# Kernel optimization log

Measured on AMD Instinct MI355X. Metric: run time of the kernel, lower is better.

The kernel has to match this reference:

```python
import jax, jax.numpy as jnp
import numpy as np

_GROUP_SIZES = [4096, 2048, 1024, 8192, 512, 3072, 6144, 1024]
_K = 2048
_N = 2048


def setup_inputs() -> dict:
    key = jax.random.key(0)
    keys = jax.random.split(key, len(_GROUP_SIZES) + 1)
    inp = {}
    for i, m in enumerate(_GROUP_SIZES):
        inp[f"A{i}"] = jax.random.normal(keys[i], (m, _K), dtype=jnp.float32)
    inp["B_shared"] = jax.random.normal(keys[-1], (_K, _N), dtype=jnp.float32)
    return inp


def reference(A0, A1, A2, A3, A4, A5, A6, A7, B_shared):
    # torch: cat([a @ B for a in group_A], dim=0)
    # Concatenating ragged groups first and doing one GEMM is the same math
    # (row-block structure of matmul), expressed as a single fused contraction.
    A_cat = jnp.concatenate([A0, A1, A2, A3, A4, A5, A6, A7], axis=0)  # [M_total, K]
    return A_cat @ B_shared  # [M_total, N]
```

## Files before the change

kernel.cpp:

```cpp
#include <hip/hip_runtime.h>
#include <hip/hip_bf16.h>

using short8  = __attribute__((ext_vector_type(8))) short;
using ushort8 = __attribute__((ext_vector_type(8))) unsigned short;
using f32x4   = __attribute__((ext_vector_type(4))) float;

#define GLB(p)  ((const __attribute__((address_space(1))) void*)(p))
#define LDSP(p) ((__attribute__((address_space(3))) void*)(p))

static __device__ __forceinline__ unsigned short f2bf(float f) {
    union { float f; unsigned u; } v; v.f = f;
    unsigned u = v.u;
    u += 0x7fffu + ((u >> 16) & 1u);
    return (unsigned short)(u >> 16);
}

#define K_DIM 2048
#define N_DIM 2048
#define M_TOTAL 26112
#define N_GROUPS 8

__global__ __launch_bounds__(256) void cvt_all(
        const float* __restrict__ A0, const float* __restrict__ A1,
        const float* __restrict__ A2, const float* __restrict__ A3,
        const float* __restrict__ A4, const float* __restrict__ A5,
        const float* __restrict__ A6, const float* __restrict__ A7,
        const float* __restrict__ B,
        unsigned short* __restrict__ Acat, unsigned short* __restrict__ Bt) {
    int b   = blockIdx.x;
    int tid = threadIdx.x;
    if (b < 4096) {
        __shared__ float t[32][33];
        int bx = b & 63, by = b >> 6;
        int tx = tid & 31, ty = tid >> 5;
#pragma unroll
        for (int i = 0; i < 32; i += 8)
            t[ty + i][tx] = B[(long)(by * 32 + ty + i) * N_DIM + bx * 32 + tx];
        __syncthreads();
#pragma unroll
        for (int i = 0; i < 32; i += 8)
            Bt[(long)(bx * 32 + ty + i) * K_DIM + by * 32 + tx] = f2bf(t[tx][ty + i]);
    } else {
        int ab = b - 4096;
        const float* src; int gb;
        if      (ab < 256)  { src = A0; gb = 0;    }
        else if (ab < 384)  { src = A1; gb = 256;  }
        else if (ab < 448)  { src = A2; gb = 384;  }
        else if (ab < 960)  { src = A3; gb = 448;  }
        else if (ab < 992)  { src = A4; gb = 960;  }
        else if (ab < 1184) { src = A5; gb = 992;  }
        else if (ab < 1568) { src = A6; gb = 1184; }
        else                { src = A7; gb = 1568; }
        const float* s    = src  + (long)(ab - gb) * 16 * K_DIM;
        unsigned short* d = Acat + (long)ab * 16 * K_DIM;
#pragma unroll 4
        for (int i = 0; i < 16; ++i) {
            long off = (long)i * K_DIM + tid * 8;
            float4 x = *(const float4*)(s + off);
            float4 y = *(const float4*)(s + off + 4);
            ushort8 o;
            o[0] = f2bf(x.x); o[1] = f2bf(x.y); o[2] = f2bf(x.z); o[3] = f2bf(x.w);
            o[4] = f2bf(y.x); o[5] = f2bf(y.y); o[6] = f2bf(y.z); o[7] = f2bf(y.w);
            *(ushort8*)(d + off) = o;
        }
    }
}


#define PBAR() __builtin_amdgcn_s_barrier()
#define VMC(n)  asm volatile("s_waitcnt vmcnt(" #n ")" ::: "memory")

#define ST_A(BUF, H, L, TT)                                                        \
    __builtin_amdgcn_global_load_lds(                                              \
        GLB(aSt + (long)((H) * 128 + (L) * 64) * K_DIM + (TT) * 64),               \
        LDSP(lds + (BUF) * 32768 + (H) * 8192 + (L) * 4096 + w * 512), 16, 0, 0)
#define ST_B(BUF, H, L, TT)                                                        \
    __builtin_amdgcn_global_load_lds(                                              \
        GLB(bSt + (long)((H) * 128 + (L) * 64) * K_DIM + (TT) * 64),               \
        LDSP(lds + (BUF) * 32768 + 16384 + (H) * 8192 + (L) * 4096 + w * 512), 16, 0, 0)

#define MMQ(MH, NH, AV, BV)                                                        \
    _Pragma("unroll") for (int i = 0; i < 4; ++i)                                  \
    _Pragma("unroll") for (int j = 0; j < 2; ++j)                                  \
        acc[(MH) * 4 + i][(NH) * 2 + j] = __builtin_amdgcn_mfma_f32_16x16x32_bf16( \
            AV[i], BV[j], acc[(MH) * 4 + i][(NH) * 2 + j], 0, 0, 0);

#define TILE(BUF, T, DO1, DO2)                                                          \
    do {                                                                                \
        const unsigned short* pA = lds + (BUF) * 32768 + wm * 1024 + r16 * 64;          \
        const unsigned short* pB = lds + (BUF) * 32768 + 16384 + wn * 1024 + r16 * 64;  \
        short8 a0[4], a1[4], b00[2], b01[2], b10[2], b11[2];                            \
           \
        _Pragma("unroll") for (int i = 0; i < 4; ++i) {                                 \
            a0[i] = *(const short8*)(pA + i * 2048 + c0 * 8);                           \
            a1[i] = *(const short8*)(pA + i * 2048 + c1 * 8);                           \
        }                                                                               \
        _Pragma("unroll") for (int j = 0; j < 2; ++j) {                                 \
            b00[j] = *(const short8*)(pB + j * 4096 + c0 * 8);                          \
            b01[j] = *(const short8*)(pB + j * 4096 + c1 * 8);                          \
        }                                                                               \
        if (DO1) { ST_A((BUF) ^ 1, 1, 0, (T) + 1); ST_A((BUF) ^ 1, 1, 1, (T) + 1); }    \
        __builtin_amdgcn_s_setprio(1); MMQ(0, 0, a0, b00); MMQ(0, 0, a1, b01);          \
        __builtin_amdgcn_s_setprio(0); PBAR();                                          \
             \
        _Pragma("unroll") for (int j = 0; j < 2; ++j) {                                 \
            b10[j] = *(const short8*)(pB + 8192 + j * 4096 + c0 * 8);                   \
            b11[j] = *(const short8*)(pB + 8192 + j * 4096 + c1 * 8);                   \
        }                                                                               \
        if (DO2) { ST_A((BUF), 0, 0, (T) + 2); ST_A((BUF), 0, 1, (T) + 2); }            \
        __builtin_amdgcn_s_setprio(1); MMQ(0, 1, a0, b10); MMQ(0, 1, a1, b11);          \
        __builtin_amdgcn_s_setprio(0); PBAR();                                          \
                        \
        _Pragma("unroll") for (int i = 0; i < 4; ++i) {                                 \
            a0[i] = *(const short8*)(pA + 8192 + i * 2048 + c0 * 8);                    \
            a1[i] = *(const short8*)(pA + 8192 + i * 2048 + c1 * 8);                    \
        }                                                                               \
        if (DO2) { ST_B((BUF), 0, 0, (T) + 2); ST_B((BUF), 0, 1, (T) + 2); }            \
        __builtin_amdgcn_s_setprio(1); MMQ(1, 0, a0, b00); MMQ(1, 0, a1, b01);          \
        __builtin_amdgcn_s_setprio(0); PBAR();                                          \
               \
        if (DO2) { ST_B((BUF), 1, 0, (T) + 2); ST_B((BUF), 1, 1, (T) + 2); VMC(6); }    \
        __builtin_amdgcn_s_setprio(1); MMQ(1, 1, a0, b10); MMQ(1, 1, a1, b11);          \
        __builtin_amdgcn_s_setprio(0);                                                  \
    } while (0)

#define ST_A4(BUF, TT)                                                             \
    __builtin_amdgcn_global_load_lds(                                              \
        GLB(aSt + (long)(TT) * 64),                                                \
        LDSP(lds + (BUF) * 4096 + w * 512), 16, 0, 0)
#define ST_B4(BUF, H, L, TT)                                                       \
    __builtin_amdgcn_global_load_lds(                                              \
        GLB(bSt + (long)((H) * 128 + (L) * 64) * K_DIM + (TT) * 64),               \
        LDSP(lds + 8192 + (BUF) * 16384 + (H) * 8192 + (L) * 4096 + w * 512), 16, 0, 0)

#define MMQ4(NH, AV, BV)                                                           \
    _Pragma("unroll") for (int i = 0; i < 2; ++i)                                  \
    _Pragma("unroll") for (int j = 0; j < 2; ++j)                                  \
        acc[i][(NH) * 2 + j] = __builtin_amdgcn_mfma_f32_16x16x32_bf16(            \
            AV[i], BV[j], acc[i][(NH) * 2 + j], 0, 0, 0);

#define TILE64(BUF, T, DO2)                                                             \
    do {                                                                                \
        const unsigned short* pA = lds + (BUF) * 4096 + wm * 1024 + r16 * 64;           \
        const unsigned short* pB = lds + 8192 + (BUF) * 16384 + wn * 1024 + r16 * 64;   \
        short8 a0[2], a1[2], b00[2], b01[2], b10[2], b11[2];                            \
                                       \
        _Pragma("unroll") for (int i = 0; i < 2; ++i) {                                 \
            a0[i] = *(const short8*)(pA + i * 2048 + c0 * 8);                           \
            a1[i] = *(const short8*)(pA + i * 2048 + c1 * 8);                           \
        }                                                                               \
        _Pragma("unroll") for (int j = 0; j < 2; ++j) {                                 \
            b00[j] = *(const short8*)(pB + j * 4096 + c0 * 8);                          \
            b01[j] = *(const short8*)(pB + j * 4096 + c1 * 8);                          \
        }                                                                               \
        __builtin_amdgcn_s_setprio(1); MMQ4(0, a0, b00);                                \
        __builtin_amdgcn_s_setprio(0); PBAR();                                          \
                                                              \
        _Pragma("unroll") for (int j = 0; j < 2; ++j) {                                 \
            b10[j] = *(const short8*)(pB + 8192 + j * 4096 + c0 * 8);                   \
            b11[j] = *(const short8*)(pB + 8192 + j * 4096 + c1 * 8);                   \
        }                                                                               \
        __builtin_amdgcn_s_setprio(1); MMQ4(0, a1, b01);                                \
        __builtin_amdgcn_s_setprio(0); PBAR();                                          \
                                         \
        if (DO2) { ST_B4((BUF), 0, 0, (T) + 2); ST_B4((BUF), 0, 1, (T) + 2); }          \
        __builtin_amdgcn_s_setprio(1); MMQ4(1, a0, b10);                                \
        __builtin_amdgcn_s_setprio(0); PBAR();                                          \
            \
        if (DO2) { ST_B4((BUF), 1, 0, (T) + 2); ST_B4((BUF), 1, 1, (T) + 2);            \
                   ST_A4((BUF), (T) + 2); VMC(5); }                                     \
        __builtin_amdgcn_s_setprio(1); MMQ4(1, a1, b11);                                \
        __builtin_amdgcn_s_setprio(0);                                                  \
    } while (0)

__global__ __launch_bounds__(512, 2) void gemm8_kernel(const unsigned short* __restrict__ Acat,
                                                       const unsigned short* __restrict__ Bt,
                                                       float* __restrict__ C) {
    __shared__ unsigned short lds[65536];

    int wg  = blockIdx.x;
    int tid = threadIdx.x;
    int l   = tid & 63;
    int w   = tid >> 6;
    int wm  = w >> 2;
    int wn  = w & 3;
    int r16 = l & 15, kq = l >> 4, x = l & 7;
    int c0  = kq ^ x;
    int c1  = (4 + kq) ^ x;
    int srow = tid >> 3;
    int sq   = (tid & 7) ^ (srow & 7);

    if (wg < 768) {
        int swz = (wg & 7) * 102 + (wg >> 3);
        int mt  = swz >> 3, nt = swz & 7;
        int m0  = mt * 256, n0 = nt * 256;

        const unsigned short* aSt = Acat + (long)(m0 + srow) * K_DIM + sq * 8;
        const unsigned short* bSt = Bt   + (long)(n0 + srow) * K_DIM + sq * 8;

        f32x4 acc[8][4] = {};

        ST_A(0, 0, 0, 0); ST_A(0, 0, 1, 0); ST_A(0, 1, 0, 0); ST_A(0, 1, 1, 0);
        ST_B(0, 0, 0, 0); ST_B(0, 0, 1, 0); ST_B(0, 1, 0, 0); ST_B(0, 1, 1, 0);
        ST_A(1, 0, 0, 1); ST_A(1, 0, 1, 1);
        ST_B(1, 0, 0, 1); ST_B(1, 0, 1, 1); ST_B(1, 1, 0, 1); ST_B(1, 1, 1, 1);
        VMC(6); PBAR();

#pragma unroll 1
        for (int t = 0; t < 30; t += 2) {
            TILE(0, t, 1, 1);     PBAR();
            TILE(1, t + 1, 1, 1); PBAR();
        }
        TILE(0, 30, 1, 0); VMC(0); PBAR();
        TILE(1, 31, 0, 0);

        int orow = m0 + wm * 16 + (l >> 4) * 4;
        int ocol = n0 + wn * 16 + (l & 15);
#pragma unroll
        for (int i = 0; i < 8; ++i)
#pragma unroll
            for (int j = 0; j < 4; ++j)
#pragma unroll
                for (int q = 0; q < 4; ++q)
                    C[(long)(orow + i * 32 + q) * N_DIM + (ocol + j * 64)] = acc[i][j][q];
    } else {
        int k    = wg - 768;
        int o    = 768 + (k >> 2);
        int qh   = k & 3;
        int swz  = (o & 7) * 102 + (o >> 3);
        int mt   = swz >> 3, nt = swz & 7;
        int m0   = mt * 256 + qh * 64, n0 = nt * 256;

        const unsigned short* aSt = Acat + (long)(m0 + srow) * K_DIM + sq * 8;
        const unsigned short* bSt = Bt   + (long)(n0 + srow) * K_DIM + sq * 8;

        f32x4 acc[2][4] = {};

        ST_A4(0, 0);
        ST_B4(0, 0, 0, 0); ST_B4(0, 0, 1, 0); ST_B4(0, 1, 0, 0); ST_B4(0, 1, 1, 0);
        ST_A4(1, 1);
        ST_B4(1, 0, 0, 1); ST_B4(1, 0, 1, 1); ST_B4(1, 1, 0, 1); ST_B4(1, 1, 1, 1);
        VMC(5); PBAR();

#pragma unroll 1
        for (int t = 0; t < 30; ++t) {
            TILE64(t & 1, t, 1); PBAR();
        }
        TILE64(0, 30, 0); VMC(0); PBAR();
        TILE64(1, 31, 0);

        int orow = m0 + wm * 16 + (l >> 4) * 4;
        int ocol = n0 + wn * 16 + (l & 15);
#pragma unroll
        for (int i = 0; i < 2; ++i)
#pragma unroll
            for (int j = 0; j < 4; ++j)
#pragma unroll
                for (int q = 0; q < 4; ++q)
                    C[(long)(orow + i * 32 + q) * N_DIM + (ocol + j * 64)] = acc[i][j][q];
    }
}

__global__ void naive_gemm_kernel(const float* __restrict__ A, const float* __restrict__ B,
                                  float* __restrict__ C, int M) {
    __shared__ float As[16][16];
    __shared__ float Bs[16][17];
    int tx = threadIdx.x, ty = threadIdx.y;
    int row = blockIdx.y * 16 + ty;
    int col = blockIdx.x * 16 + tx;
    float s = 0.f;
    for (int k0 = 0; k0 < K_DIM; k0 += 16) {
        As[ty][tx] = A[(long)row * K_DIM + k0 + tx];
        Bs[ty][tx] = B[(long)(k0 + ty) * N_DIM + col];
        __syncthreads();
#pragma unroll
        for (int t = 0; t < 16; ++t) s += As[ty][t] * Bs[t][tx];
        __syncthreads();
    }
    C[(long)row * N_DIM + col] = s;
}

extern "C" void kernel_launch(void* const* d_in, const int* in_sizes, int n_in,
                              void* d_out, int out_size, void* d_ws, size_t ws_size,
                              hipStream_t stream) {
    static const int g_m[N_GROUPS]   = {4096, 2048, 1024, 8192, 512, 3072, 6144, 1024};
    static const int g_off[N_GROUPS] = {0, 4096, 6144, 7168, 15360, 15872, 18944, 25088};

    float* C = (float*)d_out;
    const size_t need = ((size_t)M_TOTAL * K_DIM + (size_t)N_DIM * K_DIM) * 2;

    if (ws_size >= need) {
        unsigned short* Acat = (unsigned short*)d_ws;
        unsigned short* Bt   = Acat + (size_t)M_TOTAL * K_DIM;

        cvt_all<<<4096 + M_TOTAL / 16, 256, 0, stream>>>(
            (const float*)d_in[0], (const float*)d_in[1], (const float*)d_in[2],
            (const float*)d_in[3], (const float*)d_in[4], (const float*)d_in[5],
            (const float*)d_in[6], (const float*)d_in[7], (const float*)d_in[8],
            Acat, Bt);

        gemm8_kernel<<<768 + 192, 512, 0, stream>>>(Acat, Bt, C);
    } else {
        for (int g = 0; g < N_GROUPS; ++g)
            naive_gemm_kernel<<<dim3(N_DIM / 16, g_m[g] / 16), dim3(16, 16), 0, stream>>>(
                (const float*)d_in[g], (const float*)d_in[8], C + (size_t)g_off[g] * N_DIM,
                g_m[g]);
    }
}
```

Before: 275.5 us.

## Collapse GEMM tile phases from four to two with explicit vmcnt waits

Restructures the per-K-tile schedule in both the 256x256 and 64x256 GEMM paths. Each tile now runs two compute phases instead of four, with all B fragment LDS reads hoisted up front and the next-tile global->LDS prefetches batched together. Explicit s_waitcnt vmcnt values are placed per phase instead of one wait at the end. This drops intra-tile barriers to cut synchronisation overhead, at the cost of more live registers, larger load bursts, and a risk that the new wait counts do not cover LDS buffer reuse correctly.

Result: no change. 278.1 us (+0.9%).

```diff
diff --git a/kernel.cpp b/kernel.cpp
--- a/kernel.cpp
+++ b/kernel.cpp
@@ -68,7 +68,9 @@
 
 
 #define PBAR() __builtin_amdgcn_s_barrier()
-#define VMC(n)  asm volatile("s_waitcnt vmcnt(" #n ")" ::: "memory")
+#define VMC_(n) asm volatile("s_waitcnt vmcnt(" #n ")" ::: "memory")
+#define VMCX(n) VMC_(n)
+#define VMC(n)  VMC_(n)
 
 #define ST_A(BUF, H, L, TT)                                                        \
     __builtin_amdgcn_global_load_lds(                                              \
@@ -85,12 +87,12 @@
         acc[(MH) * 4 + i][(NH) * 2 + j] = __builtin_amdgcn_mfma_f32_16x16x32_bf16( \
             AV[i], BV[j], acc[(MH) * 4 + i][(NH) * 2 + j], 0, 0, 0);
 
-#define TILE(BUF, T, DO1, DO2)                                                          \
+#define TILE2(BUF, T, DO1, DO2, VA, VB)                                                 \
     do {                                                                                \
         const unsigned short* pA = lds + (BUF) * 32768 + wm * 1024 + r16 * 64;          \
         const unsigned short* pB = lds + (BUF) * 32768 + 16384 + wn * 1024 + r16 * 64;  \
         short8 a0[4], a1[4], b00[2], b01[2], b10[2], b11[2];                            \
-           \
+          \
         _Pragma("unroll") for (int i = 0; i < 4; ++i) {                                 \
             a0[i] = *(const short8*)(pA + i * 2048 + c0 * 8);                           \
             a1[i] = *(const short8*)(pA + i * 2048 + c1 * 8);                           \
@@ -98,29 +100,29 @@
         _Pragma("unroll") for (int j = 0; j < 2; ++j) {                                 \
             b00[j] = *(const short8*)(pB + j * 4096 + c0 * 8);                          \
             b01[j] = *(const short8*)(pB + j * 4096 + c1 * 8);                          \
-        }                                                                               \
-        if (DO1) { ST_A((BUF) ^ 1, 1, 0, (T) + 1); ST_A((BUF) ^ 1, 1, 1, (T) + 1); }    \
-        __builtin_amdgcn_s_setprio(1); MMQ(0, 0, a0, b00); MMQ(0, 0, a1, b01);          \
-        __builtin_amdgcn_s_setprio(0); PBAR();                                          \
-             \
-        _Pragma("unroll") for (int j = 0; j < 2; ++j) {                                 \
             b10[j] = *(const short8*)(pB + 8192 + j * 4096 + c0 * 8);                   \
             b11[j] = *(const short8*)(pB + 8192 + j * 4096 + c1 * 8);                   \
         }                                                                               \
-        if (DO2) { ST_A((BUF), 0, 0, (T) + 2); ST_A((BUF), 0, 1, (T) + 2); }            \
-        __builtin_amdgcn_s_setprio(1); MMQ(0, 1, a0, b10); MMQ(0, 1, a1, b11);          \
+        if (DO1) { ST_A((BUF) ^ 1, 1, 0, (T) + 1); ST_A((BUF) ^ 1, 1, 1, (T) + 1); }    \
+        VMCX(VA);                                                                       \
+        __builtin_amdgcn_s_setprio(1);                                                  \
+        MMQ(0, 0, a0, b00); MMQ(0, 0, a1, b01);                                         \
+        MMQ(0, 1, a0, b10); MMQ(0, 1, a1, b11);                                         \
         __builtin_amdgcn_s_setprio(0); PBAR();                                          \
-                        \
+           \
         _Pragma("unroll") for (int i = 0; i < 4; ++i) {                                 \
             a0[i] = *(const short8*)(pA + 8192 + i * 2048 + c0 * 8);                    \
             a1[i] = *(const short8*)(pA + 8192 + i * 2048 + c1 * 8);                    \
         }                                                                               \
-        if (DO2) { ST_B((BUF), 0, 0, (T) + 2); ST_B((BUF), 0, 1, (T) + 2); }            \
-        __builtin_amdgcn_s_setprio(1); MMQ(1, 0, a0, b00); MMQ(1, 0, a1, b01);          \
-        __builtin_amdgcn_s_setprio(0); PBAR();                                          \
-               \
-        if (DO2) { ST_B((BUF), 1, 0, (T) + 2); ST_B((BUF), 1, 1, (T) + 2); VMC(6); }    \
-        __builtin_amdgcn_s_setprio(1); MMQ(1, 1, a0, b10); MMQ(1, 1, a1, b11);          \
+        if (DO2) {                                                                      \
+            ST_A((BUF), 0, 0, (T) + 2); ST_A((BUF), 0, 1, (T) + 2);                     \
+            ST_B((BUF), 0, 0, (T) + 2); ST_B((BUF), 0, 1, (T) + 2);                     \
+            ST_B((BUF), 1, 0, (T) + 2); ST_B((BUF), 1, 1, (T) + 2);                     \
+        }                                                                               \
+        VMCX(VB);                                                                       \
+        __builtin_amdgcn_s_setprio(1);                                                  \
+        MMQ(1, 0, a0, b00); MMQ(1, 0, a1, b01);                                         \
+        MMQ(1, 1, a0, b10); MMQ(1, 1, a1, b11);                                         \
         __builtin_amdgcn_s_setprio(0);                                                  \
     } while (0)
 
@@ -139,12 +141,12 @@
         acc[i][(NH) * 2 + j] = __builtin_amdgcn_mfma_f32_16x16x32_bf16(            \
             AV[i], BV[j], acc[i][(NH) * 2 + j], 0, 0, 0);
 
-#define TILE64(BUF, T, DO2)                                                             \
+#define TILE64_2(BUF, T, DO2, VB)                                                       \
     do {                                                                                \
         const unsigned short* pA = lds + (BUF) * 4096 + wm * 1024 + r16 * 64;           \
         const unsigned short* pB = lds + 8192 + (BUF) * 16384 + wn * 1024 + r16 * 64;   \
         short8 a0[2], a1[2], b00[2], b01[2], b10[2], b11[2];                            \
-                                       \
+                                          \
         _Pragma("unroll") for (int i = 0; i < 2; ++i) {                                 \
             a0[i] = *(const short8*)(pA + i * 2048 + c0 * 8);                           \
             a1[i] = *(const short8*)(pA + i * 2048 + c1 * 8);                           \
@@ -152,24 +154,19 @@
         _Pragma("unroll") for (int j = 0; j < 2; ++j) {                                 \
             b00[j] = *(const short8*)(pB + j * 4096 + c0 * 8);                          \
             b01[j] = *(const short8*)(pB + j * 4096 + c1 * 8);                          \
-        }                                                                               \
-        __builtin_amdgcn_s_setprio(1); MMQ4(0, a0, b00);                                \
-        __builtin_amdgcn_s_setprio(0); PBAR();                                          \
-                                                              \
-        _Pragma("unroll") for (int j = 0; j < 2; ++j) {                                 \
             b10[j] = *(const short8*)(pB + 8192 + j * 4096 + c0 * 8);                   \
             b11[j] = *(const short8*)(pB + 8192 + j * 4096 + c1 * 8);                   \
         }                                                                               \
-        __builtin_amdgcn_s_setprio(1); MMQ4(0, a1, b01);                                \
-        __builtin_amdgcn_s_setprio(0); PBAR();                                          \
-                                         \
-        if (DO2) { ST_B4((BUF), 0, 0, (T) + 2); ST_B4((BUF), 0, 1, (T) + 2); }          \
-        __builtin_amdgcn_s_setprio(1); MMQ4(1, a0, b10);                                \
+        __builtin_amdgcn_s_setprio(1); MMQ4(0, a0, b00); MMQ4(0, a1, b01);              \
         __builtin_amdgcn_s_setprio(0); PBAR();                                          \
             \
-        if (DO2) { ST_B4((BUF), 1, 0, (T) + 2); ST_B4((BUF), 1, 1, (T) + 2);            \
-                   ST_A4((BUF), (T) + 2); VMC(5); }                                     \
-        __builtin_amdgcn_s_setprio(1); MMQ4(1, a1, b11);                                \
+        if (DO2) {                                                                      \
+            ST_B4((BUF), 0, 0, (T) + 2); ST_B4((BUF), 0, 1, (T) + 2);                   \
+            ST_B4((BUF), 1, 0, (T) + 2); ST_B4((BUF), 1, 1, (T) + 2);                   \
+            ST_A4((BUF), (T) + 2);                                                      \
+        }                                                                               \
+        VMCX(VB);                                                                       \
+        __builtin_amdgcn_s_setprio(1); MMQ4(1, a0, b10); MMQ4(1, a1, b11);              \
         __builtin_amdgcn_s_setprio(0);                                                  \
     } while (0)
 
@@ -208,11 +205,11 @@
 
 #pragma unroll 1
         for (int t = 0; t < 30; t += 2) {
-            TILE(0, t, 1, 1);     PBAR();
-            TILE(1, t + 1, 1, 1); PBAR();
+            TILE2(0, t, 1, 1, 8, 8);     PBAR();
+            TILE2(1, t + 1, 1, 1, 8, 8); PBAR();
         }
-        TILE(0, 30, 1, 0); VMC(0); PBAR();
-        TILE(1, 31, 0, 0);
+        TILE2(0, 30, 1, 0, 8, 2); PBAR();
+        TILE2(1, 31, 0, 0, 0, 0);
 
         int orow = m0 + wm * 16 + (l >> 4) * 4;
         int ocol = n0 + wn * 16 + (l & 15);
@@ -244,10 +241,10 @@
 
 #pragma unroll 1
         for (int t = 0; t < 30; ++t) {
-            TILE64(t & 1, t, 1); PBAR();
+            TILE64_2(t & 1, t, 1, 5); PBAR();
         }
-        TILE64(0, 30, 0); VMC(0); PBAR();
-        TILE64(1, 31, 0);
+        TILE64_2(0, 30, 0, 0); PBAR();
+        TILE64_2(1, 31, 0, 0);
 
         int orow = m0 + wm * 16 + (l >> 4) * 4;
         int ocol = n0 + wn * 16 + (l & 15);
```
